# Optimization experiments

Measured on AMD Instinct MI355X. Metric: run time of the kernel, lower is better.

## Reference

```python
import jax, jax.numpy as jnp
import numpy as np

NUM_ATT_HEADS = 8
NUM_LAYERS = 12
NUM_HEADS = NUM_ATT_HEADS * NUM_LAYERS  # 96
EDGE_HID = 256 // NUM_ATT_HEADS  # 32
NUM_EDGES = 1536
NUM_SPATIAL = 512
NUM_EDGE_DIS = 128
MULTI_HOP = 5


def setup_inputs() -> dict:
    key = jax.random.key(0)
    ks = jax.random.split(key, 8)
    B, N = 16, 128
    attn_bias = jax.random.normal(ks[0], (B, N + 1, N + 1), dtype=jnp.float32)
    spatial_pos = jax.random.randint(ks[1], (B, N, N), 0, NUM_SPATIAL)
    node_attr = jax.random.normal(ks[2], (B, N, 8), dtype=jnp.float32)
    edge_input = jax.random.randint(ks[3], (B, N, N, MULTI_HOP, 3), 0, NUM_EDGES)
    # learned parameters (embedding tables); padding_idx=0 rows zeroed
    edge_enc_w = jax.random.normal(ks[4], (NUM_EDGES + 1, EDGE_HID), dtype=jnp.float32) * 0.02
    edge_enc_w = edge_enc_w.at[0].set(0.0)
    edge_dis_w = jax.random.normal(ks[5], (NUM_EDGE_DIS * EDGE_HID * NUM_HEADS, 1), dtype=jnp.float32) * 0.02
    spatial_enc_w = jax.random.normal(ks[6], (NUM_SPATIAL + 10, NUM_HEADS), dtype=jnp.float32) * 0.02
    spatial_enc_w = spatial_enc_w.at[0].set(0.0)
    virt_w = jax.random.normal(ks[7], (1, NUM_HEADS), dtype=jnp.float32) * 0.02
    return {"attn_bias": attn_bias, "spatial_pos": spatial_pos, "node_attr": node_attr,
            "edge_input": edge_input, "edge_enc_w": edge_enc_w, "edge_dis_w": edge_dis_w,
            "spatial_enc_w": spatial_enc_w, "virt_w": virt_w}


def reference(attn_bias, spatial_pos, node_attr, edge_input, edge_enc_w, edge_dis_w, spatial_enc_w, virt_w):
    B, N = node_attr.shape[:2]
    H = NUM_HEADS
    g = jnp.broadcast_to(attn_bias[:, None], (B, H, N + 1, N + 1))
    # spatial position bias: [B,N,N,H] -> [B,H,N,N]
    spb = spatial_enc_w[spatial_pos].transpose(0, 3, 1, 2)
    g = g.at[:, :, 1:, 1:].add(spb)
    # graph-token virtual distance
    t = virt_w.reshape(1, H, 1)
    g = g.at[:, :, 1:, 0].add(t)
    g = g.at[:, :, 0, :].add(t)
    # hop-count normalizer
    sp = jnp.where(spatial_pos == 0, 1, spatial_pos)
    sp = jnp.where(sp > 1, sp - 1, sp)
    sp = jnp.clip(sp, 0, MULTI_HOP)
    # edge encoding: gather + mean over edge-feature axis -> [B,N,N,D,EDGE_HID]
    ei = edge_enc_w[edge_input[:, :, :, :MULTI_HOP, :]].mean(-2)
    max_dist = ei.shape[-2]
    # per-distance projection EDGE_HID -> H (the torch bmm over flattened dims)
    W = edge_dis_w.reshape(-1, EDGE_HID, H)[:max_dist]  # [D,EDGE_HID,H]
    eh = jnp.einsum('bnmdk,dkh->bnmdh', ei, W)  # [B,N,N,D,H]
    eb = eh.sum(-2) / sp.astype(ei.dtype)[..., None]  # [B,N,N,H]
    g = g.at[:, :, 1:, 1:].add(eb.transpose(0, 3, 1, 2))
    g = g + attn_bias[:, None]
    g = g.reshape(B, NUM_LAYERS, NUM_ATT_HEADS, N + 1, N + 1).transpose(1, 0, 2, 3, 4)
    return g
```

## Files before the change

kernel.cpp:

```cpp
#include <hip/hip_runtime.h>
#include <hip/hip_bf16.h>

#define NH 96
#define NE 1537
#define ND 5
#define NN 128
#define NB 16
#define NP1 129
#define OUT_PLANE (NP1 * NP1)

__device__ __forceinline__ float bflo(unsigned u) { return __uint_as_float(u << 16); }
__device__ __forceinline__ float bfhi(unsigned u) { return __uint_as_float(u & 0xffff0000u); }

__global__ __launch_bounds__(256) void k_build_M(
    const float* __restrict__ E, const float* __restrict__ Wd,
    unsigned short* __restrict__ M) {
  int o = blockIdx.x * 256 + threadIdx.x;
  if (o >= ND * NE * 24) return;
  int h4 = o % 24;
  int r  = o / 24;
  int e  = r % NE;
  int d  = r / NE;
  const float* __restrict__ Er = E + e * 32;
  const float4* __restrict__ Wp = (const float4*)(Wd + d * 32 * NH + h4 * 4);
  float4 acc = {0.f, 0.f, 0.f, 0.f};
#pragma unroll 8
  for (int k = 0; k < 32; ++k) {
    float ev = Er[k];
    float4 w = Wp[k * 24];
    acc.x = fmaf(ev, w.x, acc.x);
    acc.y = fmaf(ev, w.y, acc.y);
    acc.z = fmaf(ev, w.z, acc.z);
    acc.w = fmaf(ev, w.w, acc.w);
  }
  const float av[4] = {acc.x, acc.y, acc.z, acc.w};
  unsigned rb[4];
#pragma unroll
  for (int c = 0; c < 4; ++c) {
    unsigned u = __float_as_uint(av[c]);
    rb[c] = (u + 0x7fffu + ((u >> 16) & 1u)) >> 16;
  }
  const int half = (h4 >= 12);
  unsigned short* mp = M + (size_t)(r * 2 + half) * 64 + (h4 - half * 12) * 4;
  uint2 pk;
  pk.x = rb[0] | (rb[1] << 16);
  pk.y = rb[2] | (rb[3] << 16);
  *(uint2*)mp = pk;
}

__global__ __launch_bounds__(256, 4) void k_interior(
    const float* __restrict__ ab, const int* __restrict__ spos,
    const int* __restrict__ eidx, const float* __restrict__ spw,
    const unsigned short* __restrict__ M, float* __restrict__ out) {
  const int half = blockIdx.x & 1;
  const int jt   = blockIdx.x >> 1;
  const int n  = blockIdx.y;
  const int b  = blockIdx.z;
  const int i  = n + 1;
  const int j0 = jt * 32;

  __shared__ int   s_idx[480];
  __shared__ int   s_sp[32];
  __shared__ float s_eb[32][49];
  __shared__ float s_pad[7000];

  const int tid = threadIdx.x;
  if (tid == 0) { volatile float* vp = s_pad; vp[0] = 0.f; }

  const int pairbase = (b * NN + n) * NN + j0;
  if (tid < 120) {
    ((int4*)s_idx)[tid] = ((const int4*)(eidx + (size_t)pairbase * 15))[tid];
  }
  if (tid >= 128 && tid < 160) s_sp[tid - 128] = spos[pairbase + (tid - 128)];
  __syncthreads();

  const int p = tid >> 3;
  const int q = tid & 7;

  if (q < 6) {
    float acc[8];
#pragma unroll
    for (int c = 0; c < 8; ++c) acc[c] = 0.f;

    const int* mi = s_idx + p * 15;
#pragma unroll
    for (int g = 0; g < 15; ++g) {
      const int d = g / 3;
      const int e = mi[g];
      const uint4 w = *(const uint4*)(M + ((size_t)((d * NE + e) * 2 + half)) * 64 + q * 8);
      acc[0] += bflo(w.x); acc[1] += bfhi(w.x);
      acc[2] += bflo(w.y); acc[3] += bfhi(w.y);
      acc[4] += bflo(w.z); acc[5] += bfhi(w.z);
      acc[6] += bflo(w.w); acc[7] += bfhi(w.w);
    }

    const int spn = s_sp[p];
    const int spc = min(max(spn - 1, 1), 5);
    const float scale = 1.0f / (3.0f * (float)spc);
    const float4* __restrict__ sr = (const float4*)(spw + spn * NH + half * 48 + q * 8);
    float4 s0 = sr[0], s1 = sr[1];
    const float sv[8] = {s0.x, s0.y, s0.z, s0.w, s1.x, s1.y, s1.z, s1.w};
#pragma unroll
    for (int c = 0; c < 8; ++c) s_eb[p][q * 8 + c] = acc[c] * scale + sv[c];
  }
  __syncthreads();

  const int jl = tid & 31;
  const int hb = tid >> 5;
  const float a2v = 2.0f * ab[(b * NP1 + i) * NP1 + 1 + j0 + jl];
  const int obase = i * NP1 + 1 + j0 + jl;
#pragma unroll
  for (int c = 0; c < 6; ++c) {
    const int hl = hb * 6 + c;
    const int h  = half * 48 + hl;
    out[((h >> 3) * 128 + b * 8 + (h & 7)) * OUT_PLANE + obase] = s_eb[jl][hl] + a2v;
  }
}

__global__ __launch_bounds__(256) void k_boundary(
    const float* __restrict__ ab, const float* __restrict__ virt,
    float* __restrict__ out) {
  const int bh = blockIdx.x;
  const int b = bh / NH;
  const int h = bh % NH;
  const float t = virt[h];
  const int tid = threadIdx.x;
  const int base = ((h >> 3) * 128 + b * 8 + (h & 7)) * OUT_PLANE;
  if (tid < NP1) {
    out[base + tid] = 2.f * ab[(b * NP1) * NP1 + tid] + t;
  }
  if (tid < NN) {
    const int i = tid + 1;
    out[base + i * NP1] = 2.f * ab[(b * NP1 + i) * NP1] + t;
  }
}

extern "C" void kernel_launch(void* const* d_in, const int* in_sizes, int n_in,
                              void* d_out, int out_size, void* d_ws, size_t ws_size,
                              hipStream_t stream) {
  const float* ab   = (const float*)d_in[0];
  const int*   spos = (const int*)d_in[1];
  const int*   eidx = (const int*)d_in[3];
  const float* eenc = (const float*)d_in[4];
  const float* edis = (const float*)d_in[5];
  const float* spw  = (const float*)d_in[6];
  const float* virt = (const float*)d_in[7];
  float* out = (float*)d_out;

  unsigned short* M = (unsigned short*)d_ws;

  const int totM = ND * NE * 24;
  k_build_M<<<(totM + 255) / 256, 256, 0, stream>>>(eenc, edis, M);
  k_interior<<<dim3(8, NN, NB), 256, 0, stream>>>(ab, spos, eidx, spw, M, out);
  k_boundary<<<NB * NH, 256, 0, stream>>>(ab, virt, out);
}
```

Baseline: 213.8 us.

## Precompute gather byte offsets, batch loads, and vectorize interior output stores

The index staging now turns edge indices into byte offsets into the bf16 projection table, so the gather loop does no address arithmetic. All 15 gather loads are issued before any accumulation to raise memory-level parallelism, and accumulation uses packed float2 vectors. The output phase is remapped so each thread writes float4 vectors along j and reads attn_bias as float4. Because output rows start at an odd offset (1+j0 into a 129-wide row), these vector accesses are only 4-byte aligned, which is why the vector type is declared with aligned(4).

```diff
diff --git a/kernel.cpp b/kernel.cpp
--- a/kernel.cpp
+++ b/kernel.cpp
@@ -8,6 +8,9 @@
 #define NB 16
 #define NP1 129
 #define OUT_PLANE (NP1 * NP1)
+
+typedef float f4 __attribute__((ext_vector_type(4), aligned(4)));
+typedef float f2 __attribute__((ext_vector_type(2)));
 
 __device__ __forceinline__ float bflo(unsigned u) { return __uint_as_float(u << 16); }
 __device__ __forceinline__ float bfhi(unsigned u) { return __uint_as_float(u & 0xffff0000u); }
@@ -69,7 +72,18 @@
 
   const int pairbase = (b * NN + n) * NN + j0;
   if (tid < 120) {
-    ((int4*)s_idx)[tid] = ((const int4*)(eidx + (size_t)pairbase * 15))[tid];
+    int4 raw = ((const int4*)(eidx + (size_t)pairbase * 15))[tid];
+    const int ev[4] = {raw.x, raw.y, raw.z, raw.w};
+    const int kk = tid * 4;
+    int4 sc;
+    int* scp = (int*)&sc;
+#pragma unroll
+    for (int c = 0; c < 4; ++c) {
+      const int g = (kk + c) % 15;
+      const int d = g / 3;
+      scp[c] = ((d * NE + ev[c]) * 2 + half) * 128;
+    }
+    ((int4*)s_idx)[tid] = sc;
   }
   if (tid >= 128 && tid < 160) s_sp[tid - 128] = spos[pairbase + (tid - 128)];
   __syncthreads();
@@ -78,42 +92,68 @@
   const int q = tid & 7;
 
   if (q < 6) {
-    float acc[8];
+    const char* __restrict__ Mb = (const char*)M;
+    const unsigned qoff = q * 16;
+
+    unsigned off[15];
 #pragma unroll
-    for (int c = 0; c < 8; ++c) acc[c] = 0.f;
+    for (int g = 0; g < 15; ++g) off[g] = (unsigned)s_idx[p * 15 + g] + qoff;
 
-    const int* mi = s_idx + p * 15;
+    uint4 w[15];
+#pragma unroll
+    for (int g = 0; g < 15; ++g) w[g] = *(const uint4*)(Mb + off[g]);
+
+    f2 acc2[4];
+#pragma unroll
+    for (int c = 0; c < 4; ++c) acc2[c] = f2{0.f, 0.f};
 #pragma unroll
     for (int g = 0; g < 15; ++g) {
-      const int d = g / 3;
-      const int e = mi[g];
-      const uint4 w = *(const uint4*)(M + ((size_t)((d * NE + e) * 2 + half)) * 64 + q * 8);
-      acc[0] += bflo(w.x); acc[1] += bfhi(w.x);
-      acc[2] += bflo(w.y); acc[3] += bfhi(w.y);
-      acc[4] += bflo(w.z); acc[5] += bfhi(w.z);
-      acc[6] += bflo(w.w); acc[7] += bfhi(w.w);
+      const unsigned dw[4] = {w[g].x, w[g].y, w[g].z, w[g].w};
+#pragma unroll
+      for (int c = 0; c < 4; ++c) {
+        f2 v;
+        v.x = bflo(dw[c]);
+        v.y = bfhi(dw[c]);
+        acc2[c] += v;
+      }
     }
 
     const int spn = s_sp[p];
     const int spc = min(max(spn - 1, 1), 5);
     const float scale = 1.0f / (3.0f * (float)spc);
-    const float4* __restrict__ sr = (const float4*)(spw + spn * NH + half * 48 + q * 8);
-    float4 s0 = sr[0], s1 = sr[1];
-    const float sv[8] = {s0.x, s0.y, s0.z, s0.w, s1.x, s1.y, s1.z, s1.w};
-#pragma unroll
-    for (int c = 0; c < 8; ++c) s_eb[p][q * 8 + c] = acc[c] * scale + sv[c];
+    const f4* __restrict__ sr = (const f4*)(spw + spn * NH + half * 48 + q * 8);
+    f4 s0 = sr[0], s1 = sr[1];
+    float* eb = &s_eb[p][q * 8];
+    eb[0] = acc2[0].x * scale + s0.x;
+    eb[1] = acc2[0].y * scale + s0.y;
+    eb[2] = acc2[1].x * scale + s0.z;
+    eb[3] = acc2[1].y * scale + s0.w;
+    eb[4] = acc2[2].x * scale + s1.x;
+    eb[5] = acc2[2].y * scale + s1.y;
+    eb[6] = acc2[3].x * scale + s1.z;
+    eb[7] = acc2[3].y * scale + s1.w;
   }
   __syncthreads();
 
-  const int jl = tid & 31;
-  const int hb = tid >> 5;
-  const float a2v = 2.0f * ab[(b * NP1 + i) * NP1 + 1 + j0 + jl];
-  const int obase = i * NP1 + 1 + j0 + jl;
+  if (tid < 192) {
+    const int h = tid >> 2;
+    const int a = tid & 3;
+    const int hh = half * 48 + h;
+    float* __restrict__ op =
+        out + (size_t)((hh >> 3) * 128 + b * 8 + (hh & 7)) * OUT_PLANE
+            + i * NP1 + 1 + j0;
+    const float* __restrict__ ar = ab + (b * NP1 + i) * NP1 + 1 + j0;
 #pragma unroll
-  for (int c = 0; c < 6; ++c) {
-    const int hl = hb * 6 + c;
-    const int h  = half * 48 + hl;
-    out[((h >> 3) * 128 + b * 8 + (h & 7)) * OUT_PLANE + obase] = s_eb[jl][hl] + a2v;
+    for (int s = 0; s < 2; ++s) {
+      const int jo = a * 4 + s * 16;
+      f4 av = *(const f4*)(ar + jo);
+      f4 v;
+      v.x = fmaf(2.f, av.x, s_eb[jo + 0][h]);
+      v.y = fmaf(2.f, av.y, s_eb[jo + 1][h]);
+      v.z = fmaf(2.f, av.z, s_eb[jo + 2][h]);
+      v.w = fmaf(2.f, av.w, s_eb[jo + 3][h]);
+      *(f4*)(op + jo) = v;
+    }
   }
 }
 
@@ -125,7 +165,7 @@
   const int h = bh % NH;
   const float t = virt[h];
   const int tid = threadIdx.x;
-  const int base = ((h >> 3) * 128 + b * 8 + (h & 7)) * OUT_PLANE;
+  const size_t base = (size_t)((h >> 3) * 128 + b * 8 + (h & 7)) * OUT_PLANE;
   if (tid < NP1) {
     out[base + tid] = 2.f * ab[(b * NP1) * NP1 + tid] + t;
   }
```

New measurement: 214.9 us. About the same (+0.5%).
